# Kernel tuning notes

Hardware: AMD Instinct MI355X
Metric: run time of the kernel (lower is better)

The kernel has to match this reference:

```python
import jax, jax.numpy as jnp
import numpy as np

K = 3
S = 1
C_IN = 64
C_OUT = 128

def setup_inputs() -> dict:
    key = jax.random.key(0)
    k1, k2, k3 = jax.random.split(key, 3)
    x = jax.random.normal(k1, (16, C_IN, 256, 256), dtype=jnp.float32)
    weight = jax.random.normal(k2, (C_OUT, C_IN, K, K), dtype=jnp.float32)
    bias = jax.random.normal(k3, (C_OUT,), dtype=jnp.float32)
    return {"x": x, "weight": weight, "bias": bias}

def reference(x, weight, bias):
    # SAME-style padding of k//2 on each side, stride S, output h//S x w//S
    pad = K // 2
    out = jax.lax.conv_general_dilated(
        x, weight,
        window_strides=(S, S),
        padding=[(pad, pad), (pad, pad)],
        dimension_numbers=("NCHW", "OIHW", "NCHW"),
    )
    return out + bias[None, :, None, None]
```

## Files before the change

kernel.cpp:

```cpp
#include <hip/hip_runtime.h>


typedef _Float16 half8_t __attribute__((ext_vector_type(8)));
typedef float floatx4 __attribute__((ext_vector_type(4)));

#define HH 256
#define WW 256
#define CIN 64
#define COUT 128
#define NB 16

#define ROW_LDS 8448
#define NSLOT   10

__global__ void Conv2d_wprep_kernel(const float* __restrict__ w, _Float16* __restrict__ w_t) {
    int idx = blockIdx.x * 256 + threadIdx.x;
    if (idx >= 9 * 8 * 128 * 8) return;
    const int j = idx & 7, cout = (idx >> 3) & 127, s = (idx >> 10) & 7, t = idx >> 13;
    w_t[idx] = (_Float16)w[(cout * 64 + s * 8 + j) * 9 + t];
}

__global__ __launch_bounds__(512, 2) void Conv2dManual_77695958385099_kernel(
    const float* __restrict__ x, const _Float16* __restrict__ w_t,
    const float* __restrict__ bias, float* __restrict__ out) {
    __shared__ __align__(16) unsigned char xs[NSLOT * ROW_LDS];
    __shared__ __align__(16) float esc[8][1088];
    const int tid = threadIdx.x;
    const int l = tid & 63, wvid = tid >> 6;
    const int g = l >> 4, ln = l & 15;
    const int ow0 = blockIdx.x * 64;
    const int band = blockIdx.y;
    const int n = blockIdx.z;
    const int P0 = band * 64;

    const int rw = tid >> 7;
    const int t7 = tid & 127;
    const int su = t7 & 7;
    const int cb = t7 >> 3;
    const bool isEdge = (t7 >= 120);
    const int eu = t7 - 120;

    const char* wl = (const char*)w_t + g * 2048 + (wvid * 16 + ln) * 16;
    half8_t A[2][9];
#pragma unroll
    for (int h = 0; h < 2; ++h)
#pragma unroll
        for (int tp = 0; tp < 9; ++tp)
            A[h][tp] = *(const half8_t*)(wl + h * 8192 + tp * 16384);

    const float bv = bias[wvid * 16 + ln];

    int F[4][3][2];
#pragma unroll
    for (int cgf = 0; cgf < 4; ++cgf)
#pragma unroll
        for (int kx = 0; kx < 3; ++kx)
#pragma unroll
            for (int h = 0; h < 2; ++h) {
                const int c = cgf * 16 + kx + ln;
                F[cgf][kx][h] = c * 128 + (((4 * h + g) ^ (c & 7)) << 4);
            }

    auto stage_load = [&](int pr, float4 (&ld)[8], float (&e0)[8], float (&e1)[8]) {
        const int gr = pr - 1;
        const bool vrow = ((unsigned)gr < 256u);
        if (vrow) {
            const float4* xr = (const float4*)x +
                               (((size_t)(n * 64 + su * 8)) << 14) +
                               (size_t)gr * 64 + (ow0 >> 2) + cb;
#pragma unroll
            for (int j = 0; j < 8; ++j) ld[j] = xr[(size_t)j << 14];
        } else {
#pragma unroll
            for (int j = 0; j < 8; ++j) ld[j] = (float4){0.f, 0.f, 0.f, 0.f};
        }
        if (isEdge) {
            const float* xe = x + (((size_t)(n * 64 + eu * 8)) << 16) + (size_t)gr * 256;
#pragma unroll
            for (int j = 0; j < 8; ++j) {
                e0[j] = (vrow && ow0 > 0)        ? xe[((size_t)j << 16) + ow0 - 1]  : 0.f;
                e1[j] = (vrow && ow0 + 64 < 256) ? xe[((size_t)j << 16) + ow0 + 64] : 0.f;
            }
        }
    };
    auto stage_write = [&](int pr, const float4 (&ld)[8], const float (&e0)[8],
                           const float (&e1)[8]) {
        const unsigned sb = (unsigned)(pr % NSLOT) * ROW_LDS;
#pragma unroll
        for (int k = 0; k < 4; ++k) {
            const int c = 1 + cb * 4 + k;
            half8_t hv;
#pragma unroll
            for (int j = 0; j < 8; ++j) hv[j] = (_Float16)((const float*)&ld[j])[k];
            *(half8_t*)(xs + sb + c * 128 + ((su ^ (c & 7)) << 4)) = hv;
        }
        if (isEdge) {
            half8_t h0, h1;
#pragma unroll
            for (int j = 0; j < 8; ++j) {
                h0[j] = (_Float16)e0[j];
                h1[j] = (_Float16)e1[j];
            }
            *(half8_t*)(xs + sb + (eu << 4)) = h0;
            *(half8_t*)(xs + sb + 65 * 128 + ((eu ^ 1) << 4)) = h1;
        }
    };

    {
        float4 ld[8]; float e0[8], e1[8];
        stage_load(P0 + rw, ld, e0, e1);
        stage_write(P0 + rw, ld, e0, e1);
        if (rw < 2) {
            stage_load(P0 + 4 + rw, ld, e0, e1);
            stage_write(P0 + 4 + rw, ld, e0, e1);
        }
    }
    asm volatile("s_waitcnt lgkmcnt(0)" ::: "memory");
    __builtin_amdgcn_s_barrier();
    __builtin_amdgcn_sched_barrier(0);

    int s0 = P0 % NSLOT;
#pragma unroll 1
    for (int it = 0; it < 16; ++it) {
        float4 ld[8]; float e0[8], e1[8];
        const int prn = P0 + it * 4 + 6 + rw;
        if (it < 15) stage_load(prn, ld, e0, e1);
        __builtin_amdgcn_sched_barrier(0);

        int roff[6];
#pragma unroll
        for (int tt = 0; tt < 6; ++tt) {
            int st = s0 + tt;
            if (st >= NSLOT) st -= NSLOT;
            roff[tt] = st * ROW_LDS;
        }

        floatx4 acc[4][4];
#pragma unroll
        for (int rr = 0; rr < 4; ++rr)
#pragma unroll
            for (int cgf = 0; cgf < 4; ++cgf) acc[rr][cgf] = (floatx4){bv, bv, bv, bv};

#pragma unroll
        for (int kx = 0; kx < 3; ++kx)
#pragma unroll
            for (int h = 0; h < 2; ++h)
#pragma unroll
                for (int cgf = 0; cgf < 4; ++cgf) {
                    const unsigned char* bp = xs + F[cgf][kx][h];
                    half8_t bt[6];
#pragma unroll
                    for (int tt = 0; tt < 6; ++tt)
                        bt[tt] = *(const half8_t*)(bp + roff[tt]);
#pragma unroll
                    for (int ky = 0; ky < 3; ++ky) {
                        const half8_t af = A[h][ky * 3 + kx];
#pragma unroll
                        for (int rr = 0; rr < 4; ++rr)
                            acc[rr][cgf] = __builtin_amdgcn_mfma_f32_16x16x32_f16(
                                bt[rr + ky], af, acc[rr][cgf], 0, 0, 0);
                    }
                }

        float* scr = &esc[wvid][0];
        float* obase = out + ((size_t)(n * 128 + wvid * 16)) * 65536 +
                       (size_t)(P0 + it * 4) * 256 + ow0;
#pragma unroll
        for (int rr = 0; rr < 4; ++rr) {
#pragma unroll
            for (int cgf = 0; cgf < 4; ++cgf)
                *(floatx4*)(scr + ln * 68 + cgf * 16 + g * 4) = acc[rr][cgf];
#pragma unroll
            for (int q = 0; q < 4; ++q) {
                const int co = q * 4 + g;
                const floatx4 v = *(const floatx4*)(scr + co * 68 + ln * 4);
                __builtin_nontemporal_store(
                    v, (floatx4*)(obase + (size_t)co * 65536 + rr * 256 + ln * 4));
            }
        }

        if (it < 15) {
            stage_write(prn, ld, e0, e1);
            asm volatile("s_waitcnt lgkmcnt(0)" ::: "memory");
            __builtin_amdgcn_s_barrier();
            __builtin_amdgcn_sched_barrier(0);
        }
        s0 += 4;
        if (s0 >= NSLOT) s0 -= NSLOT;
    }
}

__global__ __launch_bounds__(256) void Conv2d_fallback_kernel(
    const float* __restrict__ x, const float* __restrict__ w,
    const float* __restrict__ bias, float* __restrict__ out) {
    const int tx = threadIdx.x & 15, ty = threadIdx.x >> 4;
    const int ow0 = blockIdx.x * 64 + tx * 4;
    const int oh = blockIdx.y * 16 + ty;
    const int gg = blockIdx.z & 7, n = blockIdx.z >> 3;
    const int co = gg * 16;
    float acc[16][4];
#pragma unroll
    for (int c = 0; c < 16; ++c) {
        const float b = bias[co + c];
#pragma unroll
        for (int p = 0; p < 4; ++p) acc[c][p] = b;
    }
    const float* xn = x + (size_t)n * CIN * HH * WW;
    const float* wb = w + (size_t)co * CIN * 9;
    for (int ci = 0; ci < CIN; ++ci) {
        const float* xc = xn + (size_t)ci * HH * WW;
        float in[3][6];
#pragma unroll
        for (int ky = 0; ky < 3; ++ky) {
            const int iy = oh + ky - 1;
            if ((unsigned)iy < (unsigned)HH) {
                const float* row = xc + iy * WW;
                const float4 v = *(const float4*)(row + ow0);
                in[ky][1] = v.x; in[ky][2] = v.y; in[ky][3] = v.z; in[ky][4] = v.w;
                in[ky][0] = (ow0 > 0) ? row[ow0 - 1] : 0.0f;
                in[ky][5] = (ow0 < WW - 4) ? row[ow0 + 4] : 0.0f;
            } else {
#pragma unroll
                for (int j = 0; j < 6; ++j) in[ky][j] = 0.0f;
            }
        }
        const float* wc2 = wb + ci * 9;
#pragma unroll
        for (int c = 0; c < 16; ++c) {
            const float* wcc = wc2 + (size_t)c * CIN * 9;
#pragma unroll
            for (int ky = 0; ky < 3; ++ky)
#pragma unroll
                for (int kx = 0; kx < 3; ++kx) {
                    const float wv2 = wcc[ky * 3 + kx];
#pragma unroll
                    for (int p = 0; p < 4; ++p) acc[c][p] += in[ky][kx + p] * wv2;
                }
        }
    }
    const size_t hw = (size_t)HH * WW;
    float* ob = out + ((size_t)n * COUT + co) * hw + (size_t)oh * WW + ow0;
#pragma unroll
    for (int c = 0; c < 16; ++c) {
        float4 v;
        v.x = acc[c][0]; v.y = acc[c][1]; v.z = acc[c][2]; v.w = acc[c][3];
        *(float4*)(ob + (size_t)c * hw) = v;
    }
}

extern "C" void kernel_launch(void* const* d_in, const int* in_sizes, int n_in,
                              void* d_out, int out_size, void* d_ws, size_t ws_size,
                              hipStream_t stream) {
    const float* x = (const float*)d_in[0];
    const float* w = (const float*)d_in[1];
    const float* b = (const float*)d_in[2];
    float* out = (float*)d_out;

    const size_t wt_bytes = (size_t)9 * 8 * 128 * 8 * 2;

    if (ws_size >= wt_bytes) {
        _Float16* w_t = (_Float16*)d_ws;
        Conv2d_wprep_kernel<<<dim3(288), 256, 0, stream>>>(w, w_t);
        Conv2dManual_77695958385099_kernel<<<dim3(4, 4, 16), 512, 0, stream>>>(
            x, w_t, b, out);
    } else {
        dim3 grid(WW / 64, HH / 16, NB * (COUT / 16));
        Conv2d_fallback_kernel<<<grid, 256, 0, stream>>>(x, w, b, out);
    }
}
```

Before: 749.8 us.

## Switch conv implicit GEMM to 32x32x16 MFMA with padded LDS rows

```diff
diff --git a/kernel.cpp b/kernel.cpp
--- a/kernel.cpp
+++ b/kernel.cpp
@@ -3,6 +3,7 @@
 
 typedef _Float16 half8_t __attribute__((ext_vector_type(8)));
 typedef float floatx4 __attribute__((ext_vector_type(4)));
+typedef float floatx16 __attribute__((ext_vector_type(16)));
 
 #define HH 256
 #define WW 256
@@ -10,8 +11,8 @@
 #define COUT 128
 #define NB 16
 
-#define ROW_LDS 8448
-#define NSLOT   10
+#define ROWB  8976
+#define NSLOT 10
 
 __global__ void Conv2d_wprep_kernel(const float* __restrict__ w, _Float16* __restrict__ w_t) {
     int idx = blockIdx.x * 256 + threadIdx.x;
@@ -23,11 +24,13 @@
 __global__ __launch_bounds__(512, 2) void Conv2dManual_77695958385099_kernel(
     const float* __restrict__ x, const _Float16* __restrict__ w_t,
     const float* __restrict__ bias, float* __restrict__ out) {
-    __shared__ __align__(16) unsigned char xs[NSLOT * ROW_LDS];
-    __shared__ __align__(16) float esc[8][1088];
+    __shared__ __align__(16) unsigned char xs[NSLOT * ROWB];
+    __shared__ __align__(16) float esc[8][1056];
     const int tid = threadIdx.x;
-    const int l = tid & 63, wvid = tid >> 6;
-    const int g = l >> 4, ln = l & 15;
+    const int l = tid & 63, wv = tid >> 6;
+    const int wc = wv >> 1;
+    const int wp = wv & 1;
+    const int l31 = l & 31, hi = l >> 5;
     const int ow0 = blockIdx.x * 64;
     const int band = blockIdx.y;
     const int n = blockIdx.z;
@@ -40,26 +43,24 @@
     const bool isEdge = (t7 >= 120);
     const int eu = t7 - 120;
 
-    const char* wl = (const char*)w_t + g * 2048 + (wvid * 16 + ln) * 16;
-    half8_t A[2][9];
-#pragma unroll
-    for (int h = 0; h < 2; ++h)
-#pragma unroll
-        for (int tp = 0; tp < 9; ++tp)
-            A[h][tp] = *(const half8_t*)(wl + h * 8192 + tp * 16384);
-
-    const float bv = bias[wvid * 16 + ln];
-
-    int F[4][3][2];
-#pragma unroll
-    for (int cgf = 0; cgf < 4; ++cgf)
-#pragma unroll
-        for (int kx = 0; kx < 3; ++kx)
-#pragma unroll
-            for (int h = 0; h < 2; ++h) {
-                const int c = cgf * 16 + kx + ln;
-                F[cgf][kx][h] = c * 128 + (((4 * h + g) ^ (c & 7)) << 4);
-            }
+    const char* wl = (const char*)w_t + (wc * 32 + l31) * 16;
+    half8_t A[9][4];
+#pragma unroll
+    for (int tp = 0; tp < 9; ++tp)
+#pragma unroll
+        for (int ks = 0; ks < 4; ++ks)
+            A[tp][ks] = *(const half8_t*)(wl + (tp * 8 + ks * 2 + hi) * 2048);
+
+    const float bv = bias[wc * 32 + l31];
+
+    int RF[3][4];
+#pragma unroll
+    for (int kx = 0; kx < 3; ++kx) {
+        const int c = wp * 32 + kx + l31;
+#pragma unroll
+        for (int ks = 0; ks < 4; ++ks)
+            RF[kx][ks] = c * 136 + (((ks * 2 + hi) ^ (c & 7)) << 4);
+    }
 
     auto stage_load = [&](int pr, float4 (&ld)[8], float (&e0)[8], float (&e1)[8]) {
         const int gr = pr - 1;
@@ -85,14 +86,14 @@
     };
     auto stage_write = [&](int pr, const float4 (&ld)[8], const float (&e0)[8],
                            const float (&e1)[8]) {
-        const unsigned sb = (unsigned)(pr % NSLOT) * ROW_LDS;
+        const unsigned sb = (unsigned)(pr % NSLOT) * ROWB;
 #pragma unroll
         for (int k = 0; k < 4; ++k) {
             const int c = 1 + cb * 4 + k;
             half8_t hv;
 #pragma unroll
             for (int j = 0; j < 8; ++j) hv[j] = (_Float16)((const float*)&ld[j])[k];
-            *(half8_t*)(xs + sb + c * 128 + ((su ^ (c & 7)) << 4)) = hv;
+            *(half8_t*)(xs + sb + c * 136 + ((su ^ (c & 7)) << 4)) = hv;
         }
         if (isEdge) {
             half8_t h0, h1;
@@ -102,7 +103,7 @@
                 h1[j] = (_Float16)e1[j];
             }
             *(half8_t*)(xs + sb + (eu << 4)) = h0;
-            *(half8_t*)(xs + sb + 65 * 128 + ((eu ^ 1) << 4)) = h1;
+            *(half8_t*)(xs + sb + 65 * 136 + ((eu ^ 1) << 4)) = h1;
         }
     };
 
@@ -122,60 +123,77 @@
     int s0 = P0 % NSLOT;
 #pragma unroll 1
     for (int it = 0; it < 16; ++it) {
+        int roff[6];
+#pragma unroll
+        for (int tt = 0; tt < 6; ++tt) {
+            int st = s0 + tt;
+            if (st >= NSLOT) st -= NSLOT;
+            roff[tt] = st * ROWB;
+        }
+
+        floatx16 acc[4];
+#pragma unroll
+        for (int rr = 0; rr < 4; ++rr)
+#pragma unroll
+            for (int i = 0; i < 16; ++i) acc[rr][i] = bv;
+
+#pragma unroll
+        for (int ks = 0; ks < 4; ++ks)
+#pragma unroll
+            for (int kx = 0; kx < 3; ++kx) {
+                half8_t bt[6];
+#pragma unroll
+                for (int tt = 0; tt < 6; ++tt)
+                    bt[tt] = *(const half8_t*)(xs + RF[kx][ks] + roff[tt]);
+#pragma unroll
+                for (int ky = 0; ky < 3; ++ky) {
+                    const half8_t af = A[ky * 3 + kx][ks];
+#pragma unroll
+                    for (int rr = 0; rr < 4; ++rr)
+                        acc[rr] = __builtin_amdgcn_mfma_f32_32x32x16_f16(
+                            bt[rr + ky], af, acc[rr], 0, 0, 0);
+                }
+            }
+
+        float* scr = &esc[wv][0];
+        const int orow0 = P0 + it * 4;
+        float* obase = out + ((size_t)(n * 128 + wc * 32)) * 65536 +
+                       (size_t)orow0 * 256 + ow0 + wp * 32;
+#pragma unroll
+        for (int rr = 0; rr < 2; ++rr) {
+#pragma unroll
+            for (int q = 0; q < 4; ++q) {
+                floatx4 v = {acc[rr][q * 4], acc[rr][q * 4 + 1],
+                             acc[rr][q * 4 + 2], acc[rr][q * 4 + 3]};
+                *(floatx4*)(scr + l31 * 33 + hi * 4 + q * 8) = v;
+            }
+#pragma unroll
+            for (int p = 0; p < 4; ++p) {
+                const int co = p * 8 + (l >> 3);
+                const floatx4 vv = *(const floatx4*)(scr + co * 33 + (l & 7) * 4);
+                __builtin_nontemporal_store(
+                    vv, (floatx4*)(obase + (size_t)co * 65536 + rr * 256 + (l & 7) * 4));
+            }
+        }
+
         float4 ld[8]; float e0[8], e1[8];
         const int prn = P0 + it * 4 + 6 + rw;
         if (it < 15) stage_load(prn, ld, e0, e1);
-        __builtin_amdgcn_sched_barrier(0);
-
-        int roff[6];
-#pragma unroll
-        for (int tt = 0; tt < 6; ++tt) {
-            int st = s0 + tt;
-            if (st >= NSLOT) st -= NSLOT;
-            roff[tt] = st * ROW_LDS;
-        }
-
-        floatx4 acc[4][4];
-#pragma unroll
-        for (int rr = 0; rr < 4; ++rr)
-#pragma unroll
-            for (int cgf = 0; cgf < 4; ++cgf) acc[rr][cgf] = (floatx4){bv, bv, bv, bv};
-
-#pragma unroll
-        for (int kx = 0; kx < 3; ++kx)
-#pragma unroll
-            for (int h = 0; h < 2; ++h)
-#pragma unroll
-                for (int cgf = 0; cgf < 4; ++cgf) {
-                    const unsigned char* bp = xs + F[cgf][kx][h];
-                    half8_t bt[6];
-#pragma unroll
-                    for (int tt = 0; tt < 6; ++tt)
-                        bt[tt] = *(const half8_t*)(bp + roff[tt]);
-#pragma unroll
-                    for (int ky = 0; ky < 3; ++ky) {
-                        const half8_t af = A[h][ky * 3 + kx];
-#pragma unroll
-                        for (int rr = 0; rr < 4; ++rr)
-                            acc[rr][cgf] = __builtin_amdgcn_mfma_f32_16x16x32_f16(
-                                bt[rr + ky], af, acc[rr][cgf], 0, 0, 0);
-                    }
-                }
-
-        float* scr = &esc[wvid][0];
-        float* obase = out + ((size_t)(n * 128 + wvid * 16)) * 65536 +
-                       (size_t)(P0 + it * 4) * 256 + ow0;
-#pragma unroll
-        for (int rr = 0; rr < 4; ++rr) {
-#pragma unroll
-            for (int cgf = 0; cgf < 4; ++cgf)
-                *(floatx4*)(scr + ln * 68 + cgf * 16 + g * 4) = acc[rr][cgf];
+
+#pragma unroll
+        for (int rr = 2; rr < 4; ++rr) {
 #pragma unroll
             for (int q = 0; q < 4; ++q) {
-                const int co = q * 4 + g;
-                const floatx4 v = *(const floatx4*)(scr + co * 68 + ln * 4);
+                floatx4 v = {acc[rr][q * 4], acc[rr][q * 4 + 1],
+                             acc[rr][q * 4 + 2], acc[rr][q * 4 + 3]};
+                *(floatx4*)(scr + l31 * 33 + hi * 4 + q * 8) = v;
+            }
+#pragma unroll
+            for (int p = 0; p < 4; ++p) {
+                const int co = p * 8 + (l >> 3);
+                const floatx4 vv = *(const floatx4*)(scr + co * 33 + (l & 7) * 4);
                 __builtin_nontemporal_store(
-                    v, (floatx4*)(obase + (size_t)co * 65536 + rr * 256 + ln * 4));
+                    vv, (floatx4*)(obase + (size_t)co * 65536 + rr * 256 + (l & 7) * 4));
             }
         }
 
```

New measurement: 837.7 us. 1.12x slower.
